# Performance work log

Measured on AMD Instinct MI355X. Metric: run time of the kernel, lower is better.

## Reference

```python
import jax, jax.numpy as jnp
import numpy as np

N_NODES = 25000
N_HEDGES = 12500
NNZ = 400000
C_IN = 128
HID = 256
HEADS = 4
DH = HID // HEADS  # 64
NQ = 1             # number_queries
LN_EPS = 1e-5


def _layer_norm(x, g, b):
    m = jnp.mean(x, axis=-1, keepdims=True)
    v = jnp.mean((x - m) ** 2, axis=-1, keepdims=True)
    return (x - m) * jax.lax.rsqrt(v + LN_EPS) * g + b


def _block(x_src, src, tgt, n_tgt, K, Qw, V, ln0_g, ln0_b, ln1_g, ln1_b, W1, W2):
    """AllSetTransformerBlock: segment-softmax multi-head attention + LN/MLP.

    x_src: [N_src, C]; K,V: [H, C, DH]; Qw: [H, NQ, DH]; src,tgt: [E] int.
    torch.sparse.softmax over dim=1 == softmax over each target's incident
    sources (unspecified entries are -inf), so a segment softmax is exact.
    """
    xK = jnp.einsum('nc,hcd->hnd', x_src, K)        # [H, N, DH]
    alpha = jnp.einsum('hqd,hnd->nhq', Qw, xK)      # [N, H, NQ]
    a = alpha[src]                                   # [E, H, NQ] gather per incidence
    m = jax.ops.segment_max(a, tgt, num_segments=n_tgt)
    e = jnp.exp(a - m[tgt])
    den = jax.ops.segment_sum(e, tgt, num_segments=n_tgt)
    attn = e / den[tgt]                              # [E, H, NQ]
    v = jnp.einsum('nc,hcd->nhd', x_src, V)[src]     # [E, H, DH]
    w = attn[:, :, :, None] * v[:, :, None, :]       # [E, H, NQ, DH]
    out = jax.ops.segment_sum(w, tgt, num_segments=n_tgt)  # [T, H, NQ, DH]
    out = out + Qw[None]                             # residual with queries
    out = out.transpose(0, 2, 1, 3).reshape(n_tgt, NQ, HID)
    x = _layer_norm(out, ln0_g, ln0_b)
    h = jnp.maximum(x @ W1, 0.0) @ W2                # MLP: Linear-ReLU-Linear, no bias
    x = _layer_norm(x + jnp.maximum(h, 0.0), ln1_g, ln1_b)
    return x.sum(axis=1)                             # [T, HID]


def setup_inputs() -> dict:
    key = jax.random.key(0)
    ks = jax.random.split(key, 12)
    # injective linear-congruential index generation -> unique (node, hedge) pairs,
    # matching a coalesced sparse incidence matrix
    P = 15485863
    lin = (np.arange(NNZ, dtype=np.int64) * P) % (N_NODES * N_HEDGES)
    node_idx = jnp.asarray(lin // N_HEDGES, dtype=jnp.int64)
    hedge_idx = jnp.asarray(lin % N_HEDGES, dtype=jnp.int64)
    s = 0.05
    w = lambda k, shape: jax.random.normal(k, shape, jnp.float32) * s
    d = {
        'x0': jax.random.normal(ks[0], (N_NODES, C_IN), jnp.float32),
        'node_idx': node_idx,
        'hedge_idx': hedge_idx,
        'n_hedges': N_HEDGES,
        'v2e_K': w(ks[1], (HEADS, C_IN, DH)),
        'v2e_Q': w(ks[2], (HEADS, NQ, DH)),
        'v2e_V': w(ks[3], (HEADS, C_IN, DH)),
        'v2e_W1': w(ks[4], (HID, HID)),
        'v2e_W2': w(ks[5], (HID, HID)),
        'v2e_ln0_g': jnp.ones(HID, jnp.float32), 'v2e_ln0_b': jnp.zeros(HID, jnp.float32),
        'v2e_ln1_g': jnp.ones(HID, jnp.float32), 'v2e_ln1_b': jnp.zeros(HID, jnp.float32),
        'e2v_K': w(ks[6], (HEADS, HID, DH)),
        'e2v_Q': w(ks[7], (HEADS, NQ, DH)),
        'e2v_V': w(ks[8], (HEADS, HID, DH)),
        'e2v_W1': w(ks[9], (HID, HID)),
        'e2v_W2': w(ks[10], (HID, HID)),
        'e2v_ln0_g': jnp.ones(HID, jnp.float32), 'e2v_ln0_b': jnp.zeros(HID, jnp.float32),
        'e2v_ln1_g': jnp.ones(HID, jnp.float32), 'e2v_ln1_b': jnp.zeros(HID, jnp.float32),
    }
    return d


def reference(x0, node_idx, hedge_idx, n_hedges,
              v2e_K, v2e_Q, v2e_V, v2e_W1, v2e_W2,
              v2e_ln0_g, v2e_ln0_b, v2e_ln1_g, v2e_ln1_b,
              e2v_K, e2v_Q, e2v_V, e2v_W1, e2v_W2,
              e2v_ln0_g, e2v_ln0_b, e2v_ln1_g, e2v_ln1_b):
    n_nodes = x0.shape[0]
    # vertex -> hyperedge (neighborhood = B^T: targets are hyperedges)
    x1 = jax.nn.relu(_block(x0, node_idx, hedge_idx, n_hedges,
                            v2e_K, v2e_Q, v2e_V,
                            v2e_ln0_g, v2e_ln0_b, v2e_ln1_g, v2e_ln1_b,
                            v2e_W1, v2e_W2))
    # hyperedge -> vertex (neighborhood = B: targets are nodes)
    x0_out = jax.nn.relu(_block(x1, hedge_idx, node_idx, n_nodes,
                                e2v_K, e2v_Q, e2v_V,
                                e2v_ln0_g, e2v_ln0_b, e2v_ln1_g, e2v_ln1_b,
                                e2v_W1, e2v_W2))
    return x0_out, x1
```

## Files before the change

### kernel.cpp

```cpp
#include <hip/hip_runtime.h>
#include <hip/hip_bf16.h>

#define N_NODES_C 25000
#define N_HEDGES_C 12500
#define NNZ_C 400000
#define C_IN_C 128
#define HID_C 256
#define LN_EPS_C 1e-5f
#define CSR_STRIDE 64

typedef unsigned short ushort_t;
typedef __attribute__((ext_vector_type(8))) short short8;
typedef __attribute__((ext_vector_type(4))) float f32x4;

union U4S8 { uint4 u; short8 s; };

__device__ __forceinline__ float ldsel(const void* p, size_t i, bool f32) {
    return f32 ? ((const float*)p)[i] : __bfloat162float(((const __hip_bfloat16*)p)[i]);
}
__device__ __forceinline__ int ldidx(const void* p, size_t i, bool i64) {
    return i64 ? (int)((const long long*)p)[i] : ((const int*)p)[i];
}
__device__ __forceinline__ ushort_t bfbits(float f) {
    union { float f; unsigned u; } v; v.f = f;
    unsigned r = v.u + 0x7FFF + ((v.u >> 16) & 1);
    return (ushort_t)(r >> 16);
}
__device__ __forceinline__ float blo(unsigned u) {
    union { unsigned u; float f; } v; v.u = u << 16; return v.f;
}
__device__ __forceinline__ float bhi(unsigned u) {
    union { unsigned u; float f; } v; v.u = u & 0xFFFF0000u; return v.f;
}

#define INIT_GRID 3273
__global__ void __launch_bounds__(256)
init_kernel(const unsigned* __restrict__ x0w, const unsigned* __restrict__ idxw,
            int* __restrict__ flags, unsigned* __restrict__ cnts,
            unsigned* __restrict__ scsrh32, unsigned* __restrict__ scsrn32,
            unsigned* __restrict__ vb32, unsigned* __restrict__ ea32) {
    int bid = blockIdx.x;
    if (bid == 0) {
        __shared__ int cnt[2];
        int t = threadIdx.x;
        if (t < 2) cnt[t] = 0;
        __syncthreads();
        int c0 = 0, c1 = 0;
        for (int k = 0; k < 4; k++) {
            unsigned w = x0w[t * 4 + k];
            unsigned elo = (w >> 7) & 0xFF;
            if (elo >= 100 && elo <= 134) c0++;
            if (idxw[2 * (t * 4 + k) + 1] == 0) c1++;
        }
        atomicAdd(&cnt[0], c0);
        atomicAdd(&cnt[1], c1);
        __syncthreads();
        if (t == 0) {
            flags[0] = (cnt[0] < 512) ? 1 : 0;
            flags[1] = (cnt[1] >= 512) ? 1 : 0;
        }
        return;
    }
    int i = (bid - 1) * 256 + threadIdx.x;
    if (i < 37500) { cnts[i] = 0u; return; }
    i -= 37500;
    if (i < 400000) { scsrh32[i] = 0x61A861A8u; return; }
    i -= 400000;
    if (i < 400000) { scsrn32[i] = 0x30D430D4u; return; }
    i -= 400000;
    if (i < 128) { vb32[25000 * 128 + i] = 0u; return; }
    i -= 128;
    if (i < 4) ea32[100000 + i] = 0u;
}

#define PREP_TOTAL 364544
__global__ void prep_kernel(const void* __restrict__ K1, const void* __restrict__ Q1,
                            const void* __restrict__ V1,
                            const void* __restrict__ K2, const void* __restrict__ Q2,
                            const void* __restrict__ V2,
                            const void* __restrict__ W1a, const void* __restrict__ W2a,
                            const void* __restrict__ W1b, const void* __restrict__ W2b,
                            const void* __restrict__ G0a, const void* __restrict__ B0a,
                            const void* __restrict__ G1a, const void* __restrict__ B1a,
                            const void* __restrict__ G0b, const void* __restrict__ B0b,
                            const void* __restrict__ G1b, const void* __restrict__ B1b,
                            const int* __restrict__ flags,
                            float* __restrict__ kq1, float* __restrict__ kq2,
                            ushort_t* __restrict__ Vt1b, ushort_t* __restrict__ Vt2b,
                            ushort_t* __restrict__ W1tA, ushort_t* __restrict__ W2tA,
                            ushort_t* __restrict__ W1tB, ushort_t* __restrict__ W2tB,
                            float* __restrict__ qgb1, float* __restrict__ ep1,
                            float* __restrict__ qgb2, float* __restrict__ ep2) {
    bool f32 = flags[0] != 0;
    size_t i = (size_t)blockIdx.x * 256 + threadIdx.x;
    if (i >= PREP_TOTAL) return;
    if (i < 512) {
        int h = (int)(i >> 7), c = (int)(i & 127);
        float s = 0.f;
        for (int d = 0; d < 64; d++)
            s += ldsel(K1, (size_t)(h * 128 + c) * 64 + d, f32) * ldsel(Q1, h * 64 + d, f32);
        kq1[h * 128 + c] = s;
        return;
    }
    i -= 512;
    if (i < 1024) {
        int h = (int)(i >> 8), c = (int)(i & 255);
        float s = 0.f;
        for (int d = 0; d < 64; d++)
            s += ldsel(K2, (size_t)(h * 256 + c) * 64 + d, f32) * ldsel(Q2, h * 64 + d, f32);
        kq2[h * 256 + c] = s;
        return;
    }
    i -= 1024;
    if (i < 32768) {
        int j = (int)(i >> 7), c = (int)(i & 127);
        int h = j >> 6, d = j & 63;
        Vt1b[i] = bfbits(ldsel(V1, (size_t)(h * 128 + c) * 64 + d, f32));
        return;
    }
    i -= 32768;
    if (i < 65536) {
        int j = (int)(i >> 8), c = (int)(i & 255);
        int h = j >> 6, d = j & 63;
        Vt2b[i] = bfbits(ldsel(V2, (size_t)(h * 256 + c) * 64 + d, f32));
        return;
    }
    i -= 65536;
    if (i < 65536) { int n = (int)(i >> 8), k = (int)(i & 255);
        W1tA[i] = bfbits(ldsel(W1a, (size_t)k * 256 + n, f32)); return; }
    i -= 65536;
    if (i < 65536) { int n = (int)(i >> 8), k = (int)(i & 255);
        W2tA[i] = bfbits(ldsel(W2a, (size_t)k * 256 + n, f32)); return; }
    i -= 65536;
    if (i < 65536) { int n = (int)(i >> 8), k = (int)(i & 255);
        W1tB[i] = bfbits(ldsel(W1b, (size_t)k * 256 + n, f32)); return; }
    i -= 65536;
    if (i < 65536) { int n = (int)(i >> 8), k = (int)(i & 255);
        W2tB[i] = bfbits(ldsel(W2b, (size_t)k * 256 + n, f32)); return; }
    i -= 65536;
    {
        int which = (int)(i >> 8);
        int j = (int)(i & 255);
        const void* src; float* dst;
        switch (which) {
            case 0: src = Q1;  dst = qgb1;       break;
            case 1: src = G0a; dst = qgb1 + 256; break;
            case 2: src = B0a; dst = qgb1 + 512; break;
            case 3: src = G1a; dst = ep1;        break;
            case 4: src = B1a; dst = ep1 + 256;  break;
            case 5: src = Q2;  dst = qgb2;       break;
            case 6: src = G0b; dst = qgb2 + 256; break;
            case 7: src = B0b; dst = qgb2 + 512; break;
            case 8: src = G1b; dst = ep2;        break;
            default: src = B1b; dst = ep2 + 256;  break;
        }
        dst[j] = ldsel(src, j, f32);
    }
}

#define FILL_CHUNK 1024
#define FILL_NCHUNK ((NNZ_C + FILL_CHUNK - 1) / FILL_CHUNK)
#define HSLICE_SZ 1563
#define NSLICE_SZ 3125
__global__ void __launch_bounds__(256)
fill_kernel(const void* __restrict__ node_idx, const void* __restrict__ hedge_idx,
            const int* __restrict__ flags,
            int* __restrict__ fill_h, int* __restrict__ fill_n,
            ushort_t* __restrict__ scsr_h, ushort_t* __restrict__ scsr_n) {
    bool i64 = flags[1] != 0;
    int s = blockIdx.x & 7;
    int chunk = blockIdx.x >> 3;
    int e0 = chunk * FILL_CHUNK;
    int e1 = e0 + FILL_CHUNK; if (e1 > NNZ_C) e1 = NNZ_C;
    int hlo = s * HSLICE_SZ, hhi = hlo + HSLICE_SZ;
    int nlo = s * NSLICE_SZ, nhi = nlo + NSLICE_SZ;
    for (int e = e0 + threadIdx.x; e < e1; e += 256) {
        int nd = ldidx(node_idx, e, i64);
        int he = ldidx(hedge_idx, e, i64);
        if (he >= hlo && he < hhi) {
            int p = atomicAdd(&fill_h[he], 1);
            if (p < CSR_STRIDE) scsr_h[(he << 6) + p] = (ushort_t)nd;
        }
        if (nd >= nlo && nd < nhi) {
            int p = atomicAdd(&fill_n[nd], 1);
            if (p < CSR_STRIDE) scsr_n[(nd << 6) + p] = (ushort_t)he;
        }
    }
}

__global__ void __launch_bounds__(256)
gemm_x0_kernel(const void* __restrict__ x0, const int* __restrict__ flags,
               const ushort_t* __restrict__ Bt, ushort_t* __restrict__ C,
               int M, int K, const float* __restrict__ kq, float* __restrict__ ea) {
    __shared__ ushort_t As[64 * 72];
    __shared__ ushort_t Bs[128 * 72];
    __shared__ float kqs[512];
    bool f32 = flags[0] != 0;
    int tid = threadIdx.x;
    int w = tid >> 6, lane = tid & 63;
    int l15 = lane & 15, kg = lane >> 4;
    int wr = w >> 1, wc = w & 1;
    int row0 = blockIdx.x * 64, col0 = blockIdx.y * 128;
    bool doEa = (blockIdx.y == 0);
    kqs[tid] = kq[tid];
    kqs[256 + tid] = kq[256 + tid];
    __syncthreads();
    f32x4 acc[2][4] = {{{0.f,0.f,0.f,0.f},{0.f,0.f,0.f,0.f},{0.f,0.f,0.f,0.f},{0.f,0.f,0.f,0.f}},
                       {{0.f,0.f,0.f,0.f},{0.f,0.f,0.f,0.f},{0.f,0.f,0.f,0.f},{0.f,0.f,0.f,0.f}}};
    float hd[2][4] = {{0.f,0.f,0.f,0.f},{0.f,0.f,0.f,0.f}};
    int r_ = tid >> 3, ch = tid & 7;
    for (int k0 = 0; k0 < K; k0 += 64) {
#pragma unroll
        for (int p = 0; p < 2; p++) {
            int r = p * 32 + r_;
            uint4 av = {0u,0u,0u,0u};
            int gr = row0 + r;
            if (gr < M) {
                float fv[8];
                if (!f32) {
                    av = *(const uint4*)((const ushort_t*)x0 + (size_t)gr * K + k0 + ch * 8);
                    if (doEa) {
                        unsigned* uw = (unsigned*)&av;
#pragma unroll
                        for (int jj = 0; jj < 4; jj++) { fv[2 * jj] = blo(uw[jj]); fv[2 * jj + 1] = bhi(uw[jj]); }
                    }
                } else {
                    const float* ap = (const float*)x0 + (size_t)gr * K + k0 + ch * 8;
                    float4 f0 = *(const float4*)ap;
                    float4 f1 = *(const float4*)(ap + 4);
                    av.x = (unsigned)bfbits(f0.x) | ((unsigned)bfbits(f0.y) << 16);
                    av.y = (unsigned)bfbits(f0.z) | ((unsigned)bfbits(f0.w) << 16);
                    av.z = (unsigned)bfbits(f1.x) | ((unsigned)bfbits(f1.y) << 16);
                    av.w = (unsigned)bfbits(f1.z) | ((unsigned)bfbits(f1.w) << 16);
                    if (doEa) {
                        fv[0] = f0.x; fv[1] = f0.y; fv[2] = f0.z; fv[3] = f0.w;
                        fv[4] = f1.x; fv[5] = f1.y; fv[6] = f1.z; fv[7] = f1.w;
                    }
                }
                if (doEa) {
                    int c = k0 + ch * 8;
#pragma unroll
                    for (int h = 0; h < 4; h++) {
                        float s = 0.f;
#pragma unroll
                        for (int j = 0; j < 8; j++) s += fv[j] * kqs[h * 128 + c + j];
                        hd[p][h] += s;
                    }
                }
            }
            *(uint4*)&As[r * 72 + ch * 8] = av;
        }
#pragma unroll
        for (int p = 0; p < 4; p++) {
            int i = p * 256 + tid;
            int r2 = i >> 3, c2 = i & 7;
            uint4 bv = *(const uint4*)(Bt + (size_t)(col0 + r2) * K + k0 + c2 * 8);
            *(uint4*)&Bs[r2 * 72 + c2 * 8] = bv;
        }
        __syncthreads();
#pragma unroll
        for (int kk = 0; kk < 2; kk++) {
            U4S8 a0_, a1_;
            a0_.u = *(const uint4*)&As[(32 * wr + l15) * 72 + kk * 32 + kg * 8];
            a1_.u = *(const uint4*)&As[(32 * wr + 16 + l15) * 72 + kk * 32 + kg * 8];
#pragma unroll
            for (int n = 0; n < 4; n++) {
                U4S8 b; b.u = *(const uint4*)&Bs[(64 * wc + 16 * n + l15) * 72 + kk * 32 + kg * 8];
                acc[0][n] = __builtin_amdgcn_mfma_f32_16x16x32_bf16(a0_.s, b.s, acc[0][n], 0, 0, 0);
                acc[1][n] = __builtin_amdgcn_mfma_f32_16x16x32_bf16(a1_.s, b.s, acc[1][n], 0, 0, 0);
            }
        }
        __syncthreads();
    }
#pragma unroll
    for (int m = 0; m < 2; m++) {
#pragma unroll
        for (int n = 0; n < 4; n++) {
#pragma unroll
            for (int rr = 0; rr < 4; rr++) {
                int row = row0 + 32 * wr + 16 * m + kg * 4 + rr;
                if (row < M)
                    C[(size_t)row * 256 + col0 + 64 * wc + 16 * n + l15] = bfbits(acc[m][n][rr]);
            }
        }
    }
    if (doEa) {
#pragma unroll
        for (int p = 0; p < 2; p++) {
#pragma unroll
            for (int msk = 1; msk < 8; msk <<= 1) {
                hd[p][0] += __shfl_xor(hd[p][0], msk);
                hd[p][1] += __shfl_xor(hd[p][1], msk);
                hd[p][2] += __shfl_xor(hd[p][2], msk);
                hd[p][3] += __shfl_xor(hd[p][3], msk);
            }
            if (ch == 0) {
                int row = row0 + p * 32 + r_;
                if (row < M) {
                    float4 o;
                    o.x = __expf(hd[p][0]); o.y = __expf(hd[p][1]);
                    o.z = __expf(hd[p][2]); o.w = __expf(hd[p][3]);
                    *(float4*)(ea + (size_t)row * 4) = o;
                }
            }
        }
    }
}

__global__ void __launch_bounds__(512)
fused_mlp_ln_kernel(const ushort_t* __restrict__ A, const ushort_t* __restrict__ W1t,
                    const ushort_t* __restrict__ W2t, const float* __restrict__ ep,
                    float* __restrict__ outF, int M,
                    const ushort_t* __restrict__ Vt2b, const float* __restrict__ kq,
                    ushort_t* __restrict__ vbOut, float* __restrict__ eaOut,
                    unsigned* __restrict__ zrow, float* __restrict__ zea) {
    __shared__ ushort_t Bs[256 * 72];
    __shared__ ushort_t hs[64 * 264];
    __shared__ float s1s[64][4];
    __shared__ float s2s[64][4];
    __shared__ float kqs[1024];
    ushort_t* As = hs;
    int tid = threadIdx.x;
    int w = tid >> 6, lane = tid & 63;
    int l15 = lane & 15, kg = lane >> 4;
    int wr = w >> 2, wc = w & 3;
    int row0 = blockIdx.x * 64;
    bool dir1 = (Vt2b != nullptr);
    if (dir1) { kqs[tid] = kq[tid]; kqs[512 + tid] = kq[512 + tid]; }
    f32x4 acc[2][4] = {{{0.f,0.f,0.f,0.f},{0.f,0.f,0.f,0.f},{0.f,0.f,0.f,0.f},{0.f,0.f,0.f,0.f}},
                       {{0.f,0.f,0.f,0.f},{0.f,0.f,0.f,0.f},{0.f,0.f,0.f,0.f},{0.f,0.f,0.f,0.f}}};
    int r = tid >> 3, ch = tid & 7;
    for (int k0 = 0; k0 < 256; k0 += 64) {
        uint4 av = {0u,0u,0u,0u};
        int gr = row0 + r;
        if (gr < M) av = *(const uint4*)(A + (size_t)gr * 256 + k0 + ch * 8);
        *(uint4*)&As[r * 72 + ch * 8] = av;
#pragma unroll
        for (int p = 0; p < 4; p++) {
            int i = p * 512 + tid;
            int r2 = i >> 3, c2 = i & 7;
            uint4 bv = *(const uint4*)(W1t + (size_t)r2 * 256 + k0 + c2 * 8);
            *(uint4*)&Bs[r2 * 72 + c2 * 8] = bv;
        }
        __syncthreads();
#pragma unroll
        for (int kk = 0; kk < 2; kk++) {
            U4S8 a0_, a1_;
            a0_.u = *(const uint4*)&As[(32 * wr + l15) * 72 + kk * 32 + kg * 8];
            a1_.u = *(const uint4*)&As[(32 * wr + 16 + l15) * 72 + kk * 32 + kg * 8];
#pragma unroll
            for (int n = 0; n < 4; n++) {
                U4S8 b; b.u = *(const uint4*)&Bs[(64 * wc + 16 * n + l15) * 72 + kk * 32 + kg * 8];
                acc[0][n] = __builtin_amdgcn_mfma_f32_16x16x32_bf16(a0_.s, b.s, acc[0][n], 0, 0, 0);
                acc[1][n] = __builtin_amdgcn_mfma_f32_16x16x32_bf16(a1_.s, b.s, acc[1][n], 0, 0, 0);
            }
        }
        __syncthreads();
    }
#pragma unroll
    for (int m = 0; m < 2; m++) {
#pragma unroll
        for (int n = 0; n < 4; n++) {
#pragma unroll
            for (int rr = 0; rr < 4; rr++) {
                int br = 32 * wr + 16 * m + kg * 4 + rr;
                hs[br * 264 + 64 * wc + 16 * n + l15] = bfbits(fmaxf(acc[m][n][rr], 0.f));
                acc[m][n][rr] = 0.f;
            }
        }
    }
    __syncthreads();
    for (int k0 = 0; k0 < 256; k0 += 64) {
#pragma unroll
        for (int p = 0; p < 4; p++) {
            int i = p * 512 + tid;
            int r2 = i >> 3, c2 = i & 7;
            uint4 bv = *(const uint4*)(W2t + (size_t)r2 * 256 + k0 + c2 * 8);
            *(uint4*)&Bs[r2 * 72 + c2 * 8] = bv;
        }
        __syncthreads();
#pragma unroll
        for (int kk = 0; kk < 2; kk++) {
            U4S8 a0_, a1_;
            a0_.u = *(const uint4*)&hs[(32 * wr + l15) * 264 + k0 + kk * 32 + kg * 8];
            a1_.u = *(const uint4*)&hs[(32 * wr + 16 + l15) * 264 + k0 + kk * 32 + kg * 8];
#pragma unroll
            for (int n = 0; n < 4; n++) {
                U4S8 b; b.u = *(const uint4*)&Bs[(64 * wc + 16 * n + l15) * 72 + kk * 32 + kg * 8];
                acc[0][n] = __builtin_amdgcn_mfma_f32_16x16x32_bf16(a0_.s, b.s, acc[0][n], 0, 0, 0);
                acc[1][n] = __builtin_amdgcn_mfma_f32_16x16x32_bf16(a1_.s, b.s, acc[1][n], 0, 0, 0);
            }
        }
        __syncthreads();
    }
    float ym[2][4][4];
#pragma unroll
    for (int m = 0; m < 2; m++) {
#pragma unroll
        for (int rr = 0; rr < 4; rr++) {
            int br = 32 * wr + 16 * m + kg * 4 + rr;
            int grow = row0 + br;
            float ls1 = 0.f;
#pragma unroll
            for (int n = 0; n < 4; n++) {
                int col = 64 * wc + 16 * n + l15;
                float xv = 0.f;
                if (grow < M) xv = blo((unsigned)A[(size_t)grow * 256 + col]);
                float yv = xv + fmaxf(acc[m][n][rr], 0.f);
                ym[m][n][rr] = yv;
                ls1 += yv;
            }
#pragma unroll
            for (int msk = 1; msk < 16; msk <<= 1) ls1 += __shfl_xor(ls1, msk);
            if (l15 == 0) s1s[br][wc] = ls1;
        }
    }
    __syncthreads();
    float mean_[2][4];
#pragma unroll
    for (int m = 0; m < 2; m++) {
#pragma unroll
        for (int rr = 0; rr < 4; rr++) {
            int br = 32 * wr + 16 * m + kg * 4 + rr;
            float mn = (s1s[br][0] + s1s[br][1] + s1s[br][2] + s1s[br][3]) * (1.f / 256.f);
            mean_[m][rr] = mn;
            float ls2 = 0.f;
#pragma unroll
            for (int n = 0; n < 4; n++) {
                float d = ym[m][n][rr] - mn;
                ls2 += d * d;
            }
#pragma unroll
            for (int msk = 1; msk < 16; msk <<= 1) ls2 += __shfl_xor(ls2, msk);
            if (l15 == 0) s2s[br][wc] = ls2;
        }
    }
    __syncthreads();
#pragma unroll
    for (int m = 0; m < 2; m++) {
#pragma unroll
        for (int rr = 0; rr < 4; rr++) {
            int br = 32 * wr + 16 * m + kg * 4 + rr;
            int grow = row0 + br;
            float var = (s2s[br][0] + s2s[br][1] + s2s[br][2] + s2s[br][3]) * (1.f / 256.f);
            float rs = rsqrtf(var + LN_EPS_C);
#pragma unroll
            for (int n = 0; n < 4; n++) {
                int col = 64 * wc + 16 * n + l15;
                float rv = (ym[m][n][rr] - mean_[m][rr]) * rs * ep[col] + ep[256 + col];
                rv = fmaxf(rv, 0.f);
                if (grow < M) outF[(size_t)grow * 256 + col] = rv;
                if (dir1) hs[br * 264 + col] = bfbits(rv);
            }
        }
    }
    if (!dir1) return;
#pragma unroll
    for (int m = 0; m < 2; m++)
#pragma unroll
        for (int n = 0; n < 4; n++)
#pragma unroll
            for (int rr = 0; rr < 4; rr++) acc[m][n][rr] = 0.f;
    __syncthreads();
    if (blockIdx.x == 0) {
        if (tid < 128) zrow[tid] = 0u;
        else if (tid < 132) zea[tid - 128] = 0.f;
    }
    {
        int rrow = tid >> 3, rch = tid & 7;
        float h0 = 0.f, h1 = 0.f, h2 = 0.f, h3 = 0.f;
#pragma unroll
        for (int q = 0; q < 4; q++) {
            uint4 xv = *(const uint4*)&hs[rrow * 264 + rch * 32 + q * 8];
            const unsigned* uw = (const unsigned*)&xv;
#pragma unroll
            for (int jj = 0; jj < 4; jj++) {
                float xl = blo(uw[jj]), xh = bhi(uw[jj]);
                int c = rch * 32 + q * 8 + jj * 2;
                h0 += xl * kqs[c]       + xh * kqs[c + 1];
                h1 += xl * kqs[256 + c] + xh * kqs[256 + c + 1];
                h2 += xl * kqs[512 + c] + xh * kqs[512 + c + 1];
                h3 += xl * kqs[768 + c] + xh * kqs[768 + c + 1];
            }
        }
#pragma unroll
        for (int msk = 1; msk < 8; msk <<= 1) {
            h0 += __shfl_xor(h0, msk); h1 += __shfl_xor(h1, msk);
            h2 += __shfl_xor(h2, msk); h3 += __shfl_xor(h3, msk);
        }
        int grow = row0 + rrow;
        if (rch == 0 && grow < M) {
            float4 o;
            o.x = __expf(h0); o.y = __expf(h1); o.z = __expf(h2); o.w = __expf(h3);
            *(float4*)(eaOut + (size_t)grow * 4) = o;
        }
    }
    for (int k0 = 0; k0 < 256; k0 += 64) {
#pragma unroll
        for (int p = 0; p < 4; p++) {
            int i = p * 512 + tid;
            int r2 = i >> 3, c2 = i & 7;
            uint4 bv = *(const uint4*)(Vt2b + (size_t)r2 * 256 + k0 + c2 * 8);
            *(uint4*)&Bs[r2 * 72 + c2 * 8] = bv;
        }
        __syncthreads();
#pragma unroll
        for (int kk = 0; kk < 2; kk++) {
            U4S8 a0_, a1_;
            a0_.u = *(const uint4*)&hs[(32 * wr + l15) * 264 + k0 + kk * 32 + kg * 8];
            a1_.u = *(const uint4*)&hs[(32 * wr + 16 + l15) * 264 + k0 + kk * 32 + kg * 8];
#pragma unroll
            for (int n = 0; n < 4; n++) {
                U4S8 b; b.u = *(const uint4*)&Bs[(64 * wc + 16 * n + l15) * 72 + kk * 32 + kg * 8];
                acc[0][n] = __builtin_amdgcn_mfma_f32_16x16x32_bf16(a0_.s, b.s, acc[0][n], 0, 0, 0);
                acc[1][n] = __builtin_amdgcn_mfma_f32_16x16x32_bf16(a1_.s, b.s, acc[1][n], 0, 0, 0);
            }
        }
        __syncthreads();
    }
#pragma unroll
    for (int m = 0; m < 2; m++) {
#pragma unroll
        for (int n = 0; n < 4; n++) {
#pragma unroll
            for (int rr = 0; rr < 4; rr++) {
                int row = row0 + 32 * wr + 16 * m + kg * 4 + rr;
                if (row < M)
                    vbOut[(size_t)row * 256 + 64 * wc + 16 * n + l15] = bfbits(acc[m][n][rr]);
            }
        }
    }
}

#define DECL_BANKD(B) float e##B##0, e##B##1, e##B##2, e##B##3; \
                      uint2 u##B##0, u##B##1, u##B##2, u##B##3;
#define ISSUED1(B, n, sl) { int _o = __shfl(myidx, (sl)) << 9; \
    u##B##n = *(const uint2*)(vbL + _o); \
    e##B##n = *(const float*)(eaL + (_o >> 5)); }
#define ISSUED4(B, base) ISSUED1(B,0,(base)) ISSUED1(B,1,(base)+1) ISSUED1(B,2,(base)+2) ISSUED1(B,3,(base)+3)
#define EATD1(B, n) { \
    float wgt = e##B##n; \
    den += wgt; \
    a0 += wgt * blo(u##B##n.x); a1 += wgt * bhi(u##B##n.x); \
    a2 += wgt * blo(u##B##n.y); a3 += wgt * bhi(u##B##n.y); }
#define EATD4(B) EATD1(B,0) EATD1(B,1) EATD1(B,2) EATD1(B,3)

__global__ void __launch_bounds__(256)
attn_ln_kernel(const int* __restrict__ cnts, const ushort_t* __restrict__ scsr,
               const char* __restrict__ eaB, const char* __restrict__ vbB,
               const float* __restrict__ qgb, uint2* __restrict__ xlnbf2) {
    int wid = (blockIdx.x << 2) + (threadIdx.x >> 6);
    int lane = threadIdx.x & 63;
    const char* vbL = vbB + (lane << 3);
    const char* eaL = eaB + ((lane >> 4) << 2);
    int cnt = cnts[wid];
    if (cnt > CSR_STRIDE) cnt = CSR_STRIDE;
    int myidx = (int)scsr[(wid << 6) + lane];
    float a0 = 0.f, a1 = 0.f, a2 = 0.f, a3 = 0.f, den = 0.f;
    int kr = (cnt + 3) & ~3;
    DECL_BANKD(A)
    DECL_BANKD(B)
    if (kr > 0) { ISSUED4(A, 0) }
    for (int k = 0; k < kr; k += 8) {
        int kb = k + 4;
        bool hasB = kb < kr;
        if (hasB) { ISSUED4(B, kb) }
        EATD4(A)
        int ka = k + 8;
        if (ka < kr) { ISSUED4(A, ka) }
        if (hasB) { EATD4(B) }
    }
    float inv = (den > 0.f) ? (1.f / den) : 0.f;
    int c0i = lane << 2;
    float o0 = a0 * inv + qgb[c0i];
    float o1 = a1 * inv + qgb[c0i + 1];
    float o2 = a2 * inv + qgb[c0i + 2];
    float o3 = a3 * inv + qgb[c0i + 3];
    float part = o0 + o1 + o2 + o3;
#pragma unroll
    for (int m = 32; m; m >>= 1) part += __shfl_xor(part, m);
    float mean = part * (1.f / 256.f);
    float d0 = o0 - mean, d1 = o1 - mean, d2 = o2 - mean, d3 = o3 - mean;
    float p2 = d0 * d0 + d1 * d1 + d2 * d2 + d3 * d3;
#pragma unroll
    for (int m = 32; m; m >>= 1) p2 += __shfl_xor(p2, m);
    float rs = rsqrtf(p2 * (1.f / 256.f) + LN_EPS_C);
    float r0 = d0 * rs * qgb[256 + c0i] + qgb[512 + c0i];
    float r1 = d1 * rs * qgb[256 + c0i + 1] + qgb[512 + c0i + 1];
    float r2 = d2 * rs * qgb[256 + c0i + 2] + qgb[512 + c0i + 2];
    float r3 = d3 * rs * qgb[256 + c0i + 3] + qgb[512 + c0i + 3];
    uint2 outw;
    outw.x = ((unsigned)bfbits(r1) << 16) | bfbits(r0);
    outw.y = ((unsigned)bfbits(r3) << 16) | bfbits(r2);
    xlnbf2[(size_t)wid * 64 + lane] = outw;
}

#define OFF_KQ1   0
#define OFF_KQ2   2048
#define OFF_QGB1  6144
#define OFF_EP1   9216
#define OFF_QGB2  11264
#define OFF_EP2   14336
#define OFF_EA    16384
#define OFF_VT1B  416512
#define OFF_VT2B  482048
#define OFF_W1TA  613120
#define OFF_W2TA  744192
#define OFF_W1TB  875264
#define OFF_W2TB  1006336
#define OFF_VB    1137408
#define OFF_XLNBF 13937920
#define OFF_FLAGS 45937920
#define OFF_FILLH 45937952
#define OFF_FILLN 45987952
#define OFF_SCSRH 46087952
#define OFF_SCSRN 47687952

extern "C" void kernel_launch(void* const* d_in, const int* in_sizes, int n_in,
                              void* d_out, int out_size, void* d_ws, size_t ws_size,
                              hipStream_t stream) {
    const void* x0        = d_in[0];
    const void* node_idx  = d_in[1];
    const void* hedge_idx = d_in[2];
    const void* v2e_K  = d_in[4];
    const void* v2e_Q  = d_in[5];
    const void* v2e_V  = d_in[6];
    const void* v2e_W1 = d_in[7];
    const void* v2e_W2 = d_in[8];
    const void* v2e_ln0_g = d_in[9];
    const void* v2e_ln0_b = d_in[10];
    const void* v2e_ln1_g = d_in[11];
    const void* v2e_ln1_b = d_in[12];
    const void* e2v_K  = d_in[13];
    const void* e2v_Q  = d_in[14];
    const void* e2v_V  = d_in[15];
    const void* e2v_W1 = d_in[16];
    const void* e2v_W2 = d_in[17];
    const void* e2v_ln0_g = d_in[18];
    const void* e2v_ln0_b = d_in[19];
    const void* e2v_ln1_g = d_in[20];
    const void* e2v_ln1_b = d_in[21];

    float* out = (float*)d_out;
    float* out_x0 = out;
    float* out_x1 = out + (size_t)N_NODES_C * HID_C;

    char* base = (char*)d_ws;
    float*    kq1   = (float*)(base + OFF_KQ1);
    float*    kq2   = (float*)(base + OFF_KQ2);
    float*    qgb1  = (float*)(base + OFF_QGB1);
    float*    ep1   = (float*)(base + OFF_EP1);
    float*    qgb2  = (float*)(base + OFF_QGB2);
    float*    ep2   = (float*)(base + OFF_EP2);
    float*    ea    = (float*)(base + OFF_EA);
    ushort_t* Vt1b  = (ushort_t*)(base + OFF_VT1B);
    ushort_t* Vt2b  = (ushort_t*)(base + OFF_VT2B);
    ushort_t* W1tA  = (ushort_t*)(base + OFF_W1TA);
    ushort_t* W2tA  = (ushort_t*)(base + OFF_W2TA);
    ushort_t* W1tB  = (ushort_t*)(base + OFF_W1TB);
    ushort_t* W2tB  = (ushort_t*)(base + OFF_W2TB);
    ushort_t* vb    = (ushort_t*)(base + OFF_VB);
    ushort_t* xlnbf = (ushort_t*)(base + OFF_XLNBF);
    int*      flags = (int*)(base + OFF_FLAGS);
    int*      fill_h = (int*)(base + OFF_FILLH);
    int*      fill_n = (int*)(base + OFF_FILLN);
    ushort_t* scsr_h = (ushort_t*)(base + OFF_SCSRH);
    ushort_t* scsr_n = (ushort_t*)(base + OFF_SCSRN);

    init_kernel<<<INIT_GRID, 256, 0, stream>>>(
        (const unsigned*)x0, (const unsigned*)node_idx, flags,
        (unsigned*)fill_h, (unsigned*)scsr_h, (unsigned*)scsr_n,
        (unsigned*)vb, (unsigned*)ea);

    prep_kernel<<<(PREP_TOTAL + 255) / 256, 256, 0, stream>>>(
        v2e_K, v2e_Q, v2e_V, e2v_K, e2v_Q, e2v_V,
        v2e_W1, v2e_W2, e2v_W1, e2v_W2,
        v2e_ln0_g, v2e_ln0_b, v2e_ln1_g, v2e_ln1_b,
        e2v_ln0_g, e2v_ln0_b, e2v_ln1_g, e2v_ln1_b,
        flags, kq1, kq2, Vt1b, Vt2b, W1tA, W2tA, W1tB, W2tB,
        qgb1, ep1, qgb2, ep2);

    fill_kernel<<<8 * FILL_NCHUNK, 256, 0, stream>>>(
        node_idx, hedge_idx, flags, fill_h, fill_n, scsr_h, scsr_n);

    gemm_x0_kernel<<<dim3((N_NODES_C + 63) / 64, 2), 256, 0, stream>>>(
        x0, flags, Vt1b, vb, N_NODES_C, C_IN_C, kq1, ea);
    attn_ln_kernel<<<N_HEDGES_C / 4, 256, 0, stream>>>(
        fill_h, scsr_h, (const char*)ea, (const char*)vb, qgb1, (uint2*)xlnbf);
    fused_mlp_ln_kernel<<<(N_HEDGES_C + 63) / 64, 512, 0, stream>>>(
        xlnbf, W1tA, W2tA, ep1, out_x1, N_HEDGES_C,
        Vt2b, kq2, vb, ea,
        (unsigned*)vb + 12500 * 128, ea + 50000);

    attn_ln_kernel<<<N_NODES_C / 4, 256, 0, stream>>>(
        fill_n, scsr_n, (const char*)ea, (const char*)vb, qgb2, (uint2*)xlnbf);
    fused_mlp_ln_kernel<<<(N_NODES_C + 63) / 64, 512, 0, stream>>>(
        xlnbf, W1tB, W2tB, ep2, out_x0, N_NODES_C,
        nullptr, nullptr, nullptr, nullptr, nullptr, nullptr);
}
```

Measured before the change: 190.9 us.

## Halve MLP row tile to 32 and register-prefetch next weight K-slab

The fused MLP/LN kernel now processes 32 rows per block instead of 64. This doubles the grid (about 391 and 782 blocks) and halves accumulator registers and shared memory. Weight tiles for the next K step are loaded into registers before the current MFMA loop runs, so global loads overlap compute. In exchange, each weight slab is loaded by twice as many blocks, roughly doubling weight reads from L2 and lowering reuse per block.

```diff
diff --git a/kernel.cpp b/kernel.cpp
--- a/kernel.cpp
+++ b/kernel.cpp
@@ -307,6 +307,17 @@
     }
 }
 
+#define LOADB4(SRC, KO) { \
+    bv0 = *(const uint4*)((SRC) + (size_t)rb * 256 + (KO) + cb * 8); \
+    bv1 = *(const uint4*)((SRC) + (size_t)(rb + 64) * 256 + (KO) + cb * 8); \
+    bv2 = *(const uint4*)((SRC) + (size_t)(rb + 128) * 256 + (KO) + cb * 8); \
+    bv3 = *(const uint4*)((SRC) + (size_t)(rb + 192) * 256 + (KO) + cb * 8); }
+#define WRITEB4() { \
+    *(uint4*)&Bs[rb * 72 + cb * 8] = bv0; \
+    *(uint4*)&Bs[(rb + 64) * 72 + cb * 8] = bv1; \
+    *(uint4*)&Bs[(rb + 128) * 72 + cb * 8] = bv2; \
+    *(uint4*)&Bs[(rb + 192) * 72 + cb * 8] = bv3; }
+
 __global__ void __launch_bounds__(512)
 fused_mlp_ln_kernel(const ushort_t* __restrict__ A, const ushort_t* __restrict__ W1t,
                     const ushort_t* __restrict__ W2t, const float* __restrict__ ep,
@@ -315,168 +326,147 @@
                     ushort_t* __restrict__ vbOut, float* __restrict__ eaOut,
                     unsigned* __restrict__ zrow, float* __restrict__ zea) {
     __shared__ ushort_t Bs[256 * 72];
-    __shared__ ushort_t hs[64 * 264];
-    __shared__ float s1s[64][4];
-    __shared__ float s2s[64][4];
+    __shared__ ushort_t hs[32 * 264];
+    __shared__ float s1s[32][4];
+    __shared__ float s2s[32][4];
     __shared__ float kqs[1024];
     ushort_t* As = hs;
     int tid = threadIdx.x;
     int w = tid >> 6, lane = tid & 63;
     int l15 = lane & 15, kg = lane >> 4;
     int wr = w >> 2, wc = w & 3;
-    int row0 = blockIdx.x * 64;
+    int row0 = blockIdx.x * 32;
     bool dir1 = (Vt2b != nullptr);
     if (dir1) { kqs[tid] = kq[tid]; kqs[512 + tid] = kq[512 + tid]; }
-    f32x4 acc[2][4] = {{{0.f,0.f,0.f,0.f},{0.f,0.f,0.f,0.f},{0.f,0.f,0.f,0.f},{0.f,0.f,0.f,0.f}},
-                       {{0.f,0.f,0.f,0.f},{0.f,0.f,0.f,0.f},{0.f,0.f,0.f,0.f},{0.f,0.f,0.f,0.f}}};
-    int r = tid >> 3, ch = tid & 7;
+    f32x4 acc[4] = {{0.f,0.f,0.f,0.f},{0.f,0.f,0.f,0.f},{0.f,0.f,0.f,0.f},{0.f,0.f,0.f,0.f}};
+    int rb = tid >> 3, cb = tid & 7;
+    bool doA = tid < 256;
+    int gr = row0 + rb;
+    uint4 av = {0u,0u,0u,0u};
+    uint4 bv0, bv1, bv2, bv3;
+    LOADB4(W1t, 0);
+    if (doA && gr < M) av = *(const uint4*)(A + (size_t)gr * 256 + cb * 8);
     for (int k0 = 0; k0 < 256; k0 += 64) {
-        uint4 av = {0u,0u,0u,0u};
-        int gr = row0 + r;
-        if (gr < M) av = *(const uint4*)(A + (size_t)gr * 256 + k0 + ch * 8);
-        *(uint4*)&As[r * 72 + ch * 8] = av;
-#pragma unroll
-        for (int p = 0; p < 4; p++) {
-            int i = p * 512 + tid;
-            int r2 = i >> 3, c2 = i & 7;
-            uint4 bv = *(const uint4*)(W1t + (size_t)r2 * 256 + k0 + c2 * 8);
-            *(uint4*)&Bs[r2 * 72 + c2 * 8] = bv;
-        }
-        __syncthreads();
+        WRITEB4();
+        if (doA) *(uint4*)&As[rb * 72 + cb * 8] = av;
+        __syncthreads();
+        if (k0 < 192) {
+            LOADB4(W1t, k0 + 64);
+            if (doA && gr < M) av = *(const uint4*)(A + (size_t)gr * 256 + (k0 + 64) + cb * 8);
+        }
 #pragma unroll
         for (int kk = 0; kk < 2; kk++) {
-            U4S8 a0_, a1_;
-            a0_.u = *(const uint4*)&As[(32 * wr + l15) * 72 + kk * 32 + kg * 8];
-            a1_.u = *(const uint4*)&As[(32 * wr + 16 + l15) * 72 + kk * 32 + kg * 8];
+            U4S8 a0_;
+            a0_.u = *(const uint4*)&As[(16 * wr + l15) * 72 + kk * 32 + kg * 8];
 #pragma unroll
             for (int n = 0; n < 4; n++) {
                 U4S8 b; b.u = *(const uint4*)&Bs[(64 * wc + 16 * n + l15) * 72 + kk * 32 + kg * 8];
-                acc[0][n] = __builtin_amdgcn_mfma_f32_16x16x32_bf16(a0_.s, b.s, acc[0][n], 0, 0, 0);
-                acc[1][n] = __builtin_amdgcn_mfma_f32_16x16x32_bf16(a1_.s, b.s, acc[1][n], 0, 0, 0);
-            }
-        }
-        __syncthreads();
-    }
-#pragma unroll
-    for (int m = 0; m < 2; m++) {
-#pragma unroll
-        for (int n = 0; n < 4; n++) {
-#pragma unroll
-            for (int rr = 0; rr < 4; rr++) {
-                int br = 32 * wr + 16 * m + kg * 4 + rr;
-                hs[br * 264 + 64 * wc + 16 * n + l15] = bfbits(fmaxf(acc[m][n][rr], 0.f));
-                acc[m][n][rr] = 0.f;
-            }
+                acc[n] = __builtin_amdgcn_mfma_f32_16x16x32_bf16(a0_.s, b.s, acc[n], 0, 0, 0);
+            }
+        }
+        __syncthreads();
+    }
+    LOADB4(W2t, 0);
+#pragma unroll
+    for (int n = 0; n < 4; n++) {
+#pragma unroll
+        for (int rr = 0; rr < 4; rr++) {
+            int br = 16 * wr + kg * 4 + rr;
+            hs[br * 264 + 64 * wc + 16 * n + l15] = bfbits(fmaxf(acc[n][rr], 0.f));
+            acc[n][rr] = 0.f;
         }
     }
     __syncthreads();
     for (int k0 = 0; k0 < 256; k0 += 64) {
-#pragma unroll
-        for (int p = 0; p < 4; p++) {
-            int i = p * 512 + tid;
-            int r2 = i >> 3, c2 = i & 7;
-            uint4 bv = *(const uint4*)(W2t + (size_t)r2 * 256 + k0 + c2 * 8);
-            *(uint4*)&Bs[r2 * 72 + c2 * 8] = bv;
-        }
-        __syncthreads();
+        WRITEB4();
+        __syncthreads();
+        if (k0 < 192) LOADB4(W2t, k0 + 64);
 #pragma unroll
         for (int kk = 0; kk < 2; kk++) {
-            U4S8 a0_, a1_;
-            a0_.u = *(const uint4*)&hs[(32 * wr + l15) * 264 + k0 + kk * 32 + kg * 8];
-            a1_.u = *(const uint4*)&hs[(32 * wr + 16 + l15) * 264 + k0 + kk * 32 + kg * 8];
+            U4S8 a0_;
+            a0_.u = *(const uint4*)&hs[(16 * wr + l15) * 264 + k0 + kk * 32 + kg * 8];
 #pragma unroll
             for (int n = 0; n < 4; n++) {
                 U4S8 b; b.u = *(const uint4*)&Bs[(64 * wc + 16 * n + l15) * 72 + kk * 32 + kg * 8];
-                acc[0][n] = __builtin_amdgcn_mfma_f32_16x16x32_bf16(a0_.s, b.s, acc[0][n], 0, 0, 0);
-                acc[1][n] = __builtin_amdgcn_mfma_f32_16x16x32_bf16(a1_.s, b.s, acc[1][n], 0, 0, 0);
-            }
-        }
-        __syncthreads();
-    }
-    float ym[2][4][4];
-#pragma unroll
-    for (int m = 0; m < 2; m++) {
-#pragma unroll
-        for (int rr = 0; rr < 4; rr++) {
-            int br = 32 * wr + 16 * m + kg * 4 + rr;
-            int grow = row0 + br;
-            float ls1 = 0.f;
-#pragma unroll
-            for (int n = 0; n < 4; n++) {
-                int col = 64 * wc + 16 * n + l15;
-                float xv = 0.f;
-                if (grow < M) xv = blo((unsigned)A[(size_t)grow * 256 + col]);
-                float yv = xv + fmaxf(acc[m][n][rr], 0.f);
-                ym[m][n][rr] = yv;
-                ls1 += yv;
-            }
-#pragma unroll
-            for (int msk = 1; msk < 16; msk <<= 1) ls1 += __shfl_xor(ls1, msk);
-            if (l15 == 0) s1s[br][wc] = ls1;
-        }
+                acc[n] = __builtin_amdgcn_mfma_f32_16x16x32_bf16(a0_.s, b.s, acc[n], 0, 0, 0);
+            }
+        }
+        __syncthreads();
+    }
+    float ym[4][4];
+#pragma unroll
+    for (int rr = 0; rr < 4; rr++) {
+        int br = 16 * wr + kg * 4 + rr;
+        int grow = row0 + br;
+        float ls1 = 0.f;
+#pragma unroll
+        for (int n = 0; n < 4; n++) {
+            int col = 64 * wc + 16 * n + l15;
+            float xv = 0.f;
+            if (grow < M) xv = blo((unsigned)A[(size_t)grow * 256 + col]);
+            float yv = xv + fmaxf(acc[n][rr], 0.f);
+            ym[n][rr] = yv;
+            ls1 += yv;
+        }
+#pragma unroll
+        for (int msk = 1; msk < 16; msk <<= 1) ls1 += __shfl_xor(ls1, msk);
+        if (l15 == 0) s1s[br][wc] = ls1;
     }
     __syncthreads();
-    float mean_[2][4];
-#pragma unroll
-    for (int m = 0; m < 2; m++) {
-#pragma unroll
-        for (int rr = 0; rr < 4; rr++) {
-            int br = 32 * wr + 16 * m + kg * 4 + rr;
-            float mn = (s1s[br][0] + s1s[br][1] + s1s[br][2] + s1s[br][3]) * (1.f / 256.f);
-            mean_[m][rr] = mn;
-            float ls2 = 0.f;
-#pragma unroll
-            for (int n = 0; n < 4; n++) {
-                float d = ym[m][n][rr] - mn;
-                ls2 += d * d;
-            }
-#pragma unroll
-            for (int msk = 1; msk < 16; msk <<= 1) ls2 += __shfl_xor(ls2, msk);
-            if (l15 == 0) s2s[br][wc] = ls2;
-        }
+    float mean_[4];
+#pragma unroll
+    for (int rr = 0; rr < 4; rr++) {
+        int br = 16 * wr + kg * 4 + rr;
+        float mn = (s1s[br][0] + s1s[br][1] + s1s[br][2] + s1s[br][3]) * (1.f / 256.f);
+        mean_[rr] = mn;
+        float ls2 = 0.f;
+#pragma unroll
+        for (int n = 0; n < 4; n++) {
+            float d = ym[n][rr] - mn;
+            ls2 += d * d;
+        }
+#pragma unroll
+        for (int msk = 1; msk < 16; msk <<= 1) ls2 += __shfl_xor(ls2, msk);
+        if (l15 == 0) s2s[br][wc] = ls2;
     }
     __syncthreads();
 #pragma unroll
-    for (int m = 0; m < 2; m++) {
-#pragma unroll
-        for (int rr = 0; rr < 4; rr++) {
-            int br = 32 * wr + 16 * m + kg * 4 + rr;
-            int grow = row0 + br;
-            float var = (s2s[br][0] + s2s[br][1] + s2s[br][2] + s2s[br][3]) * (1.f / 256.f);
-            float rs = rsqrtf(var + LN_EPS_C);
-#pragma unroll
-            for (int n = 0; n < 4; n++) {
-                int col = 64 * wc + 16 * n + l15;
-                float rv = (ym[m][n][rr] - mean_[m][rr]) * rs * ep[col] + ep[256 + col];
-                rv = fmaxf(rv, 0.f);
-                if (grow < M) outF[(size_t)grow * 256 + col] = rv;
-                if (dir1) hs[br * 264 + col] = bfbits(rv);
-            }
+    for (int rr = 0; rr < 4; rr++) {
+        int br = 16 * wr + kg * 4 + rr;
+        int grow = row0 + br;
+        float var = (s2s[br][0] + s2s[br][1] + s2s[br][2] + s2s[br][3]) * (1.f / 256.f);
+        float rs = rsqrtf(var + LN_EPS_C);
+#pragma unroll
+        for (int n = 0; n < 4; n++) {
+            int col = 64 * wc + 16 * n + l15;
+            float rv = (ym[n][rr] - mean_[rr]) * rs * ep[col] + ep[256 + col];
+            rv = fmaxf(rv, 0.f);
+            if (grow < M) outF[(size_t)grow * 256 + col] = rv;
+            if (dir1) hs[br * 264 + col] = bfbits(rv);
         }
     }
     if (!dir1) return;
 #pragma unroll
-    for (int m = 0; m < 2; m++)
-#pragma unroll
-        for (int n = 0; n < 4; n++)
-#pragma unroll
-            for (int rr = 0; rr < 4; rr++) acc[m][n][rr] = 0.f;
+    for (int n = 0; n < 4; n++)
+#pragma unroll
+        for (int rr = 0; rr < 4; rr++) acc[n][rr] = 0.f;
+    LOADB4(Vt2b, 0);
     __syncthreads();
     if (blockIdx.x == 0) {
         if (tid < 128) zrow[tid] = 0u;
         else if (tid < 132) zea[tid - 128] = 0.f;
     }
     {
-        int rrow = tid >> 3, rch = tid & 7;
+        int rrow = tid >> 4, rch = tid & 15;
         float h0 = 0.f, h1 = 0.f, h2 = 0.f, h3 = 0.f;
 #pragma unroll
-        for (int q = 0; q < 4; q++) {
-            uint4 xv = *(const uint4*)&hs[rrow * 264 + rch * 32 + q * 8];
+        for (int q = 0; q < 2; q++) {
+            uint4 xv = *(const uint4*)&hs[rrow * 264 + rch * 16 + q * 8];
             const unsigned* uw = (const unsigned*)&xv;
 #pragma unroll
             for (int jj = 0; jj < 4; jj++) {
                 float xl = blo(uw[jj]), xh = bhi(uw[jj]);
-                int c = rch * 32 + q * 8 + jj * 2;
+                int c = rch * 16 + q * 8 + jj * 2;
                 h0 += xl * kqs[c]       + xh * kqs[c + 1];
                 h1 += xl * kqs[256 + c] + xh * kqs[256 + c + 1];
                 h2 += xl * kqs[512 + c] + xh * kqs[512 + c + 1];
@@ -484,7 +474,7 @@
             }
         }
 #pragma unroll
-        for (int msk = 1; msk < 8; msk <<= 1) {
+        for (int msk = 1; msk < 16; msk <<= 1) {
             h0 += __shfl_xor(h0, msk); h1 += __shfl_xor(h1, msk);
             h2 += __shfl_xor(h2, msk); h3 += __shfl_xor(h3, msk);
         }
@@ -496,38 +486,28 @@
         }
     }
     for (int k0 = 0; k0 < 256; k0 += 64) {
-#pragma unroll
-        for (int p = 0; p < 4; p++) {
-            int i = p * 512 + tid;
-            int r2 = i >> 3, c2 = i & 7;
-            uint4 bv = *(const uint4*)(Vt2b + (size_t)r2 * 256 + k0 + c2 * 8);
-            *(uint4*)&Bs[r2 * 72 + c2 * 8] = bv;
-        }
-        __syncthreads();
+        WRITEB4();
+        __syncthreads();
+        if (k0 < 192) LOADB4(Vt2b, k0 + 64);
 #pragma unroll
         for (int kk = 0; kk < 2; kk++) {
-            U4S8 a0_, a1_;
-            a0_.u = *(const uint4*)&hs[(32 * wr + l15) * 264 + k0 + kk * 32 + kg * 8];
-            a1_.u = *(const uint4*)&hs[(32 * wr + 16 + l15) * 264 + k0 + kk * 32 + kg * 8];
+            U4S8 a0_;
+            a0_.u = *(const uint4*)&hs[(16 * wr + l15) * 264 + k0 + kk * 32 + kg * 8];
 #pragma unroll
             for (int n = 0; n < 4; n++) {
                 U4S8 b; b.u = *(const uint4*)&Bs[(64 * wc + 16 * n + l15) * 72 + kk * 32 + kg * 8];
-                acc[0][n] = __builtin_amdgcn_mfma_f32_16x16x32_bf16(a0_.s, b.s, acc[0][n], 0, 0, 0);
-                acc[1][n] = __builtin_amdgcn_mfma_f32_16x16x32_bf16(a1_.s, b.s, acc[1][n], 0, 0, 0);
-            }
-        }
-        __syncthreads();
-    }
-#pragma unroll
-    for (int m = 0; m < 2; m++) {
-#pragma unroll
-        for (int n = 0; n < 4; n++) {
-#pragma unroll
-            for (int rr = 0; rr < 4; rr++) {
-                int row = row0 + 32 * wr + 16 * m + kg * 4 + rr;
-                if (row < M)
-                    vbOut[(size_t)row * 256 + 64 * wc + 16 * n + l15] = bfbits(acc[m][n][rr]);
-            }
+                acc[n] = __builtin_amdgcn_mfma_f32_16x16x32_bf16(a0_.s, b.s, acc[n], 0, 0, 0);
+            }
+        }
+        __syncthreads();
+    }
+#pragma unroll
+    for (int n = 0; n < 4; n++) {
+#pragma unroll
+        for (int rr = 0; rr < 4; rr++) {
+            int row = row0 + 16 * wr + kg * 4 + rr;
+            if (row < M)
+                vbOut[(size_t)row * 256 + 64 * wc + 16 * n + l15] = bfbits(acc[n][rr]);
         }
     }
 }
@@ -687,14 +667,14 @@
         x0, flags, Vt1b, vb, N_NODES_C, C_IN_C, kq1, ea);
     attn_ln_kernel<<<N_HEDGES_C / 4, 256, 0, stream>>>(
         fill_h, scsr_h, (const char*)ea, (const char*)vb, qgb1, (uint2*)xlnbf);
-    fused_mlp_ln_kernel<<<(N_HEDGES_C + 63) / 64, 512, 0, stream>>>(
+    fused_mlp_ln_kernel<<<(N_HEDGES_C + 31) / 32, 512, 0, stream>>>(
         xlnbf, W1tA, W2tA, ep1, out_x1, N_HEDGES_C,
         Vt2b, kq2, vb, ea,
         (unsigned*)vb + 12500 * 128, ea + 50000);
 
     attn_ln_kernel<<<N_NODES_C / 4, 256, 0, stream>>>(
         fill_n, scsr_n, (const char*)ea, (const char*)vb, qgb2, (uint2*)xlnbf);
-    fused_mlp_ln_kernel<<<(N_NODES_C + 63) / 64, 512, 0, stream>>>(
+    fused_mlp_ln_kernel<<<(N_NODES_C + 31) / 32, 512, 0, stream>>>(
         xlnbf, W1tB, W2tB, ep2, out_x0, N_NODES_C,
         nullptr, nullptr, nullptr, nullptr, nullptr, nullptr);
 }
```

Measured after the change: 193.2 us. No clear change (+1.2%).
